# Performance work log

Hardware: AMD Instinct MI355X
Metric: run time of the kernel (lower is better)

## Reference

```python
import math
import jax, jax.numpy as jnp
import numpy as np

EMB = 768
N_HEAD = 12
B, T = 8, 1024

def setup_inputs() -> dict:
    key = jax.random.key(0)
    ks = jax.random.split(key, 5)
    x = jax.random.normal(ks[0], (B, T, EMB), dtype=jnp.float32)
    # linear params (torch nn.Linear: y = x @ W.T + b); store as [in, out] for einsum
    s1 = 1.0 / math.sqrt(EMB)
    W_attn = jax.random.uniform(ks[1], (EMB, 3 * EMB), jnp.float32, -s1, s1)
    b_attn = jax.random.uniform(ks[2], (3 * EMB,), jnp.float32, -s1, s1)
    W_proj = jax.random.uniform(ks[3], (EMB, EMB), jnp.float32, -s1, s1)
    b_proj = jax.random.uniform(ks[4], (EMB,), jnp.float32, -s1, s1)
    return {"x": x, "W_attn": W_attn, "b_attn": b_attn, "W_proj": W_proj, "b_proj": b_proj}

def reference(x, W_attn, b_attn, W_proj, b_proj):
    Bb, Tt, C = x.shape
    hd = C // N_HEAD
    qkv = x @ W_attn + b_attn                       # [B,T,3C]
    q, k, v = jnp.split(qkv, 3, axis=-1)
    # [B,T,C] -> [B,H,T,hd]
    def to_heads(t):
        return t.reshape(Bb, Tt, N_HEAD, hd).transpose(0, 2, 1, 3)
    q, k, v = to_heads(q), to_heads(k), to_heads(v)
    scale = 1.0 / math.sqrt(hd)
    scores = jnp.einsum('bhqd,bhkd->bhqk', q, k) * scale   # [B,H,T,T]
    causal = jnp.tril(jnp.ones((Tt, Tt), dtype=bool))
    scores = jnp.where(causal[None, None], scores, jnp.float32(-jnp.inf))
    attn = jax.nn.softmax(scores, axis=-1)
    y = jnp.einsum('bhqk,bhkd->bhqd', attn, v)              # [B,H,T,hd]
    y = y.transpose(0, 2, 1, 3).reshape(Bb, Tt, C)
    return y @ W_proj + b_proj
```

## Files before the change

### kernel.cpp

```cpp
#include <hip/hip_runtime.h>
#include <hip/hip_bf16.h>

typedef __hip_bfloat16 bf16;
typedef __attribute__((ext_vector_type(8))) short  bfrag;
typedef __attribute__((ext_vector_type(4))) float  facc;
typedef __attribute__((ext_vector_type(4))) short  short4v;

#define B_   8
#define T_   1024
#define C_   768
#define H_   12
#define HD_  64
#define M_   (B_ * T_)
#define N3_  (3 * C_)

#define QSCALE_ 0.18033688011112042f
#define M2_     17.312340490667562f

__device__ __forceinline__ float fexp2(float x) { return __builtin_amdgcn_exp2f(x); }

__device__ __forceinline__ void gload_lds16(const bf16* g, bf16* l) {
    __builtin_amdgcn_global_load_lds((const __attribute__((address_space(1))) void*)g,
                                     (__attribute__((address_space(3))) void*)l, 16, 0, 0);
}
__device__ __forceinline__ short bfbits(float f) {
    bf16 b = __float2bfloat16(f);
    return *reinterpret_cast<short*>(&b);
}

#define XBLK 6144
#define WABLK 1728
__global__ __launch_bounds__(256) void cvt_all_kernel(
        const float* __restrict__ x,  bf16* __restrict__ xb,
        const float* __restrict__ wa, bf16* __restrict__ wat,
        const float* __restrict__ wp, bf16* __restrict__ wpt) {
    const int bid = blockIdx.x, t = threadIdx.x;
    if (bid < XBLK) {
        const size_t i = ((size_t)bid * 256 + t) * 4;
        const float4 v = *(const float4*)(x + i);
        bf16* o = xb + i;
        o[0] = __float2bfloat16(v.x); o[1] = __float2bfloat16(v.y);
        o[2] = __float2bfloat16(v.z); o[3] = __float2bfloat16(v.w);
        return;
    }
    __shared__ float tile[32][33];
    const float* w; bf16* wt; int N, tI;
    if (bid < XBLK + WABLK) { w = wa; wt = wat; N = N3_; tI = bid - XBLK; }
    else                    { w = wp; wt = wpt; N = C_;  tI = bid - XBLK - WABLK; }
    const int ntn = N / 32;
    const int n0 = (tI % ntn) * 32, k0 = (tI / ntn) * 32;
    const int tx = t & 31, ty = t >> 5;
    for (int i = ty; i < 32; i += 8) tile[i][tx] = w[(size_t)(k0 + i) * N + n0 + tx];
    __syncthreads();
    for (int i = ty; i < 32; i += 8)
        wt[(size_t)(n0 + i) * C_ + k0 + tx] = __float2bfloat16(tile[tx][i]);
}


#define WAIT_VM(N) asm volatile("s_waitcnt vmcnt(" #N ")" ::: "memory")
#define PHASE_MID() do { __builtin_amdgcn_s_barrier();                 \
    asm volatile("s_waitcnt lgkmcnt(0)" ::: "memory");                 \
    __builtin_amdgcn_sched_barrier(0);                                 \
    __builtin_amdgcn_s_setprio(1); } while (0)
#define PHASE_END() do { __builtin_amdgcn_s_setprio(0);                \
    __builtin_amdgcn_s_barrier(); } while (0)

#define G_LOAD_A() _Pragma("unroll") for (int i = 0; i < 4; ++i) {             \
    const bf16* ar = AsC + (wrow + i * 16 + fr) * 64;                          \
    af[i][0] = *(const bfrag*)(ar + pc0);                                      \
    af[i][1] = *(const bfrag*)(ar + pc1); }

#define G_LOAD_B(CH) _Pragma("unroll") for (int j = 0; j < 2; ++j) {           \
    const bf16* br = BsC + (wcol + (CH) * 32 + j * 16 + fr) * 64;              \
    bf_[j][0] = *(const bfrag*)(br + pc0);                                     \
    bf_[j][1] = *(const bfrag*)(br + pc1); }

#define G_MFMA(CH) _Pragma("unroll") for (int i = 0; i < 4; ++i)               \
    _Pragma("unroll") for (int j = 0; j < 2; ++j) {                            \
      facc& a = acc[i][(CH) * 2 + j];                                          \
      if constexpr (SWAPPED) {                                                 \
        a = __builtin_amdgcn_mfma_f32_16x16x32_bf16(bf_[j][0], af[i][0], a, 0, 0, 0); \
        a = __builtin_amdgcn_mfma_f32_16x16x32_bf16(bf_[j][1], af[i][1], a, 0, 0, 0); \
      } else {                                                                 \
        a = __builtin_amdgcn_mfma_f32_16x16x32_bf16(af[i][0], bf_[j][0], a, 0, 0, 0); \
        a = __builtin_amdgcn_mfma_f32_16x16x32_bf16(af[i][1], bf_[j][1], a, 0, 0, 0); \
      } }

template<bool SWAPPED>
__device__ __forceinline__ void gemm192_core(
        const bf16* __restrict__ Ap, const bf16* __restrict__ Bp,
        const int m0, const int n0, bf16* smem, facc (&acc)[4][6]) {
    constexpr int KD = 768, NT = 12;
    bf16* As = smem;
    bf16* Bs = smem + 2 * 8192;
    const int t = threadIdx.x, w = t >> 6, lane = t & 63;
    const int wrow = (w >> 1) * 64;
    const int wcol = (w & 1) * 96;
    const int fr = lane & 15, quad = lane >> 4;
    const int pc0 = (quad ^ (fr & 7)) * 8;
    const int pc1 = ((quad + 4) ^ (fr & 7)) * 8;
    const int srow = t >> 3;
    const int schunk = ((t & 7) ^ (srow & 7)) * 8;
    const int sdo = srow * 64 + (t & 7) * 8;

    const bf16* Ag = Ap + (size_t)(m0 + srow) * KD + schunk;
    const bf16* Bg = Bp + (size_t)(n0 + srow) * KD + schunk;

#pragma unroll
    for (int i = 0; i < 4; ++i)
#pragma unroll
        for (int c = 0; c < 6; ++c)
#pragma unroll
            for (int r = 0; r < 4; ++r) acc[i][c][r] = 0.f;

    auto stageA = [&](bf16* dst, int k0) {
        const bf16* s = Ag + k0;
        bf16* d = dst + sdo;
#pragma unroll
        for (int r = 0; r < 4; ++r)
            gload_lds16(s + (size_t)(r * 32) * KD, d + r * 2048);
    };
    auto stageB = [&](bf16* dst, int u, int k0) {
        const bf16* s = Bg + (size_t)(u * 64) * KD + k0;
        bf16* d = dst + u * 4096 + sdo;
        gload_lds16(s, d);
        gload_lds16(s + (size_t)32 * KD, d + 2048);
    };

    stageA(As, 0);
    stageB(Bs, 0, 0); stageB(Bs, 1, 0); stageB(Bs, 2, 0);
    WAIT_VM(4);
    __builtin_amdgcn_s_barrier();

#pragma unroll 2
    for (int kt = 0; kt < NT; ++kt) {
        const int cb = kt & 1;
        const bf16* AsC = As + cb * 8192;
        const bf16* BsC = Bs + cb * 12288;
        bf16* AsN = As + (cb ^ 1) * 8192;
        bf16* BsN = Bs + (cb ^ 1) * 12288;
        const int kn = (kt + 1) * 64;
        const bool nl = kt + 1 < NT;
        bfrag af[4][2], bf_[2][2];

        G_LOAD_A();
        G_LOAD_B(0);
        if (nl) { stageA(AsN, kn); WAIT_VM(6); } else { WAIT_VM(2); }
        PHASE_MID();
        G_MFMA(0);
        PHASE_END();

        G_LOAD_B(1);
        if (nl) { stageB(BsN, 0, kn); stageB(BsN, 1, kn); WAIT_VM(8); } else { WAIT_VM(0); }
        PHASE_MID();
        G_MFMA(1);
        PHASE_END();

        G_LOAD_B(2);
        if (nl) { stageB(BsN, 2, kn); WAIT_VM(4); }
        PHASE_MID();
        G_MFMA(2);
        PHASE_END();
    }
}

__global__ __launch_bounds__(256, 2) void qkv192_kernel(
        const bf16* __restrict__ xb, const bf16* __restrict__ wat,
        const float* __restrict__ bias,
        bf16* __restrict__ Q, bf16* __restrict__ K, bf16* __restrict__ Vt) {
    extern __shared__ bf16 smem[];
    const int id = blockIdx.x;
    const int wg = (id & 7) * 96 + (id >> 3);
    const int bx = wg % 12, by = wg / 12;
    const int m0 = by * 128, n0 = bx * 192;
    const int which = n0 / C_;

    facc acc[4][6];
    if (which < 2) gemm192_core<true >(xb, wat, m0, n0, smem, acc);
    else           gemm192_core<false>(xb, wat, m0, n0, smem, acc);

    const int t = threadIdx.x, w = t >> 6, lane = t & 63;
    const int wr = (w >> 1) * 64, wc = (w & 1) * 96;
    const int fr = lane & 15, quad = lane >> 4;
    const int bb = m0 >> 10;
    if (which < 2) {
        bf16* dst = which ? K : Q;
        const float sc = which ? 1.0f : QSCALE_;
#pragma unroll
        for (int i = 0; i < 4; ++i) {
            const int tt = (m0 & 1023) + wr + i * 16 + fr;
#pragma unroll
            for (int c = 0; c < 6; ++c) {
                const int colbase = n0 + wc + c * 16 + quad * 4;
                const int cc = colbase - which * C_;
                const int h = cc >> 6, d0 = cc & 63;
                const float4 bv = *(const float4*)(bias + colbase);
                short4v pk;
                pk[0] = bfbits((acc[i][c][0] + bv.x) * sc);
                pk[1] = bfbits((acc[i][c][1] + bv.y) * sc);
                pk[2] = bfbits((acc[i][c][2] + bv.z) * sc);
                pk[3] = bfbits((acc[i][c][3] + bv.w) * sc);
                *(short4v*)(dst + ((size_t)(bb * H_ + h) * T_ + tt) * HD_ + d0) = pk;
            }
        }
    } else {
#pragma unroll
        for (int i = 0; i < 4; ++i) {
            const int tt0 = (m0 & 1023) + wr + i * 16 + quad * 4;
#pragma unroll
            for (int c = 0; c < 6; ++c) {
                const int col = n0 + wc + c * 16 + fr;
                const int cc = col - 2 * C_;
                const int h = cc >> 6, d = cc & 63;
                const float bv = bias[col];
                short4v pk;
                pk[0] = bfbits(acc[i][c][0] + bv);
                pk[1] = bfbits(acc[i][c][1] + bv);
                pk[2] = bfbits(acc[i][c][2] + bv);
                pk[3] = bfbits(acc[i][c][3] + bv);
                *(short4v*)(Vt + ((size_t)(bb * H_ + h) * HD_ + d) * T_ + tt0) = pk;
            }
        }
    }
}

__global__ __launch_bounds__(256, 2) void proj192_kernel(
        const bf16* __restrict__ y, const bf16* __restrict__ wpt,
        const float* __restrict__ bias, float* __restrict__ out) {
    extern __shared__ bf16 smem[];
    const int id = blockIdx.x;
    const int wg = (id & 7) * 32 + (id >> 3);
    const int bx = wg % 4, by = wg / 4;
    const int m0 = by * 128, n0 = bx * 192;

    facc acc[4][6];
    gemm192_core<true>(y, wpt, m0, n0, smem, acc);

    const int t = threadIdx.x, w = t >> 6, lane = t & 63;
    const int wr = (w >> 1) * 64, wc = (w & 1) * 96;
    const int fr = lane & 15, quad = lane >> 4;
#pragma unroll
    for (int i = 0; i < 4; ++i) {
        const int row = m0 + wr + i * 16 + fr;
#pragma unroll
        for (int c = 0; c < 6; ++c) {
            const int colbase = n0 + wc + c * 16 + quad * 4;
            const float4 bv = *(const float4*)(bias + colbase);
            float4 v;
            v.x = acc[i][c][0] + bv.x;
            v.y = acc[i][c][1] + bv.y;
            v.z = acc[i][c][2] + bv.z;
            v.w = acc[i][c][3] + bv.w;
            *(float4*)(out + (size_t)row * C_ + colbase) = v;
        }
    }
}

__global__ __launch_bounds__(256) void flash_attn_kernel(
        const bf16* __restrict__ Q, const bf16* __restrict__ K,
        const bf16* __restrict__ Vt, bf16* __restrict__ Y) {
    const int id   = blockIdx.x;
    const int bh   = (id & 7) * 12 + ((id >> 3) % 12);
    const int qpair = (id >> 3) / 12;
    const int t = threadIdx.x, w = t >> 6, lane = t & 63;
    const int fr = lane & 15, quad = lane >> 4, fq = quad * 8;

    __shared__ bf16 sK[2][64 * 64];
    __shared__ bf16 sVt[2][64 * 64];
    __shared__ bf16 sP[4][16][72];

    const bf16* Kbh = K  + (size_t)bh * T_ * HD_;
    const bf16* Vbh = Vt + (size_t)bh * HD_ * T_;
    const int b_ = bh / H_, h_ = bh % H_;

    const int srow = t >> 3;
    const int sgc  = ((t & 7) ^ (srow & 7)) * 8;
    const int c0   = (quad ^ (fr & 7)) * 8;

    for (int phase = 0; phase < 2; ++phase) {
        const int qt = (phase == 0) ? (15 - qpair) : qpair;
        const int q0 = qt * 64;

        const bf16* qbase = Q + ((size_t)bh * T_ + q0 + w * 16 + fr) * HD_;
        bfrag qa0 = *(const bfrag*)(qbase + fq);
        bfrag qa1 = *(const bfrag*)(qbase + 32 + fq);

        facc o[4];
        for (int nb = 0; nb < 4; ++nb) for (int r = 0; r < 4; ++r) o[nb][r] = 0.f;
        float rowl[4] = {0.f, 0.f, 0.f, 0.f};

        auto tile_step = [&](int kt, const bf16* sKp, const bf16* sVp) {
            const int k0 = kt * 64;
            facc s[4];
            for (int nb = 0; nb < 4; ++nb) for (int r = 0; r < 4; ++r) s[nb][r] = 0.f;
            for (int nb = 0; nb < 4; ++nb) {
                const bf16* kr = sKp + (nb * 16 + fr) * 64;
                bfrag kb0 = *(const bfrag*)(kr + c0);
                bfrag kb1 = *(const bfrag*)(kr + (c0 ^ 32));
                s[nb] = __builtin_amdgcn_mfma_f32_16x16x32_bf16(qa0, kb0, s[nb], 0, 0, 0);
                s[nb] = __builtin_amdgcn_mfma_f32_16x16x32_bf16(qa1, kb1, s[nb], 0, 0, 0);
            }
            const int mrow0 = q0 + w * 16 + quad * 4;
            float p[4][4];
            if (kt == qt) {
                for (int nb = 0; nb < 4; ++nb) {
                    const int n_g = k0 + nb * 16 + fr;
                    for (int r = 0; r < 4; ++r) {
                        const float a = (n_g > mrow0 + r) ? -1e30f : s[nb][r] - M2_;
                        p[nb][r] = fexp2(a);
                    }
                }
            } else {
                for (int nb = 0; nb < 4; ++nb)
                    for (int r = 0; r < 4; ++r)
                        p[nb][r] = fexp2(s[nb][r] - M2_);
            }
            for (int r = 0; r < 4; ++r)
                rowl[r] += p[0][r] + p[1][r] + p[2][r] + p[3][r];
            for (int nb = 0; nb < 4; ++nb)
                for (int r = 0; r < 4; ++r)
                    sP[w][quad * 4 + r][nb * 16 + fr] = __float2bfloat16(p[nb][r]);
            bfrag pa0 = *(const bfrag*)(&sP[w][fr][fq]);
            bfrag pa1 = *(const bfrag*)(&sP[w][fr][32 + fq]);
            for (int nb = 0; nb < 4; ++nb) {
                const bf16* vr = sVp + (nb * 16 + fr) * 64;
                bfrag vb0 = *(const bfrag*)(vr + c0);
                bfrag vb1 = *(const bfrag*)(vr + (c0 ^ 32));
                o[nb] = __builtin_amdgcn_mfma_f32_16x16x32_bf16(pa0, vb0, o[nb], 0, 0, 0);
                o[nb] = __builtin_amdgcn_mfma_f32_16x16x32_bf16(pa1, vb1, o[nb], 0, 0, 0);
            }
        };

        for (int kt = 0; kt <= qt; kt += 2) {
            const int k0 = kt * 64;
            const bool two = (kt + 1 <= qt);
            gload_lds16(Kbh + (size_t)(k0 + srow) * HD_ + sgc,      sK[0] + t * 8);
            gload_lds16(Kbh + (size_t)(k0 + 32 + srow) * HD_ + sgc, sK[0] + 2048 + t * 8);
            gload_lds16(Vbh + (size_t)srow * T_ + k0 + sgc,         sVt[0] + t * 8);
            gload_lds16(Vbh + (size_t)(srow + 32) * T_ + k0 + sgc,  sVt[0] + 2048 + t * 8);
            if (two) {
                const int k1 = k0 + 64;
                gload_lds16(Kbh + (size_t)(k1 + srow) * HD_ + sgc,      sK[1] + t * 8);
                gload_lds16(Kbh + (size_t)(k1 + 32 + srow) * HD_ + sgc, sK[1] + 2048 + t * 8);
                gload_lds16(Vbh + (size_t)srow * T_ + k1 + sgc,         sVt[1] + t * 8);
                gload_lds16(Vbh + (size_t)(srow + 32) * T_ + k1 + sgc,  sVt[1] + 2048 + t * 8);
            }
            __syncthreads();
            tile_step(kt, sK[0], sVt[0]);
            if (two) tile_step(kt + 1, sK[1], sVt[1]);
            __syncthreads();
        }

        for (int r = 0; r < 4; ++r) {
            float l = rowl[r];
            l += __shfl_xor(l, 1);
            l += __shfl_xor(l, 2);
            l += __shfl_xor(l, 4);
            l += __shfl_xor(l, 8);
            const float inv = 1.0f / l;
            const int tt = q0 + w * 16 + quad * 4 + r;
            bf16* yrow = Y + ((size_t)b_ * T_ + tt) * C_ + h_ * HD_;
            for (int nb = 0; nb < 4; ++nb)
                yrow[nb * 16 + fr] = __float2bfloat16(o[nb][r] * inv);
        }
    }
}

extern "C" void kernel_launch(void* const* d_in, const int* in_sizes, int n_in,
                              void* d_out, int out_size, void* d_ws, size_t ws_size,
                              hipStream_t stream) {
    const float* x      = (const float*)d_in[0];
    const float* W_attn = (const float*)d_in[1];
    const float* b_attn = (const float*)d_in[2];
    const float* W_proj = (const float*)d_in[3];
    const float* b_proj = (const float*)d_in[4];
    float* out = (float*)d_out;

    const size_t per = (size_t)B_ * H_ * T_ * HD_;
    bf16* Q   = (bf16*)d_ws;
    bf16* K   = Q + per;
    bf16* Vt  = K + per;
    bf16* XbY = Vt + per;
    bf16* WaT = XbY + per;
    bf16* WpT = WaT + (size_t)N3_ * C_;

    static bool s_attr = false;
    if (!s_attr) {
        hipFuncSetAttribute((const void*)qkv192_kernel,
                            hipFuncAttributeMaxDynamicSharedMemorySize, 81920);
        hipFuncSetAttribute((const void*)proj192_kernel,
                            hipFuncAttributeMaxDynamicSharedMemorySize, 81920);
        s_attr = true;
    }

    cvt_all_kernel<<<dim3(XBLK + WABLK + 576), dim3(256), 0, stream>>>(
        x, XbY, W_attn, WaT, W_proj, WpT);
    qkv192_kernel<<<dim3(768), dim3(256), 81920, stream>>>(
        XbY, WaT, b_attn, Q, K, Vt);
    flash_attn_kernel<<<dim3(768), dim3(256), 0, stream>>>(Q, K, Vt, XbY);
    proj192_kernel<<<dim3(256), dim3(256), 81920, stream>>>(
        XbY, WpT, b_proj, out);
}
```

Before: 176.2 us.

## Use 8-wave GEMM blocks with 256-row QKV tiles and rebalanced load pipeline

The shared GEMM core becomes 8-wave (512-thread) blocks, templated on rows per wave. The QKV GEMM now uses 256x192 tiles in 384 blocks, and the projection uses 128x192 tiles with half the rows per wave. Global-to-LDS staging is reorganized: all of B is issued in one phase and the wait counts are adjusted. The goal is more operand reuse per LDS tile and more waves to hide latency. The cost is 112KB of LDS for the QKV kernel, which likely limits it to one block per CU, and a fragile hand-tuned vmcnt schedule.

```diff
diff --git a/kernel.cpp b/kernel.cpp
--- a/kernel.cpp
+++ b/kernel.cpp
@@ -65,19 +65,19 @@
 #define PHASE_END() do { __builtin_amdgcn_s_setprio(0);                \
     __builtin_amdgcn_s_barrier(); } while (0)
 
-#define G_LOAD_A() _Pragma("unroll") for (int i = 0; i < 4; ++i) {             \
+#define L_A() _Pragma("unroll") for (int i = 0; i < MI; ++i) {                 \
     const bf16* ar = AsC + (wrow + i * 16 + fr) * 64;                          \
     af[i][0] = *(const bfrag*)(ar + pc0);                                      \
     af[i][1] = *(const bfrag*)(ar + pc1); }
 
-#define G_LOAD_B(CH) _Pragma("unroll") for (int j = 0; j < 2; ++j) {           \
-    const bf16* br = BsC + (wcol + (CH) * 32 + j * 16 + fr) * 64;              \
+#define L_B(P) _Pragma("unroll") for (int j = 0; j < 2; ++j) {                 \
+    const bf16* br = BsC + (wcol + ((P) * 2 + j) * 16 + fr) * 64;              \
     bf_[j][0] = *(const bfrag*)(br + pc0);                                     \
     bf_[j][1] = *(const bfrag*)(br + pc1); }
 
-#define G_MFMA(CH) _Pragma("unroll") for (int i = 0; i < 4; ++i)               \
+#define MM(P) _Pragma("unroll") for (int i = 0; i < MI; ++i)                   \
     _Pragma("unroll") for (int j = 0; j < 2; ++j) {                            \
-      facc& a = acc[i][(CH) * 2 + j];                                          \
+      facc& a = acc[i][(P) * 2 + j];                                           \
       if constexpr (SWAPPED) {                                                 \
         a = __builtin_amdgcn_mfma_f32_16x16x32_bf16(bf_[j][0], af[i][0], a, 0, 0, 0); \
         a = __builtin_amdgcn_mfma_f32_16x16x32_bf16(bf_[j][1], af[i][1], a, 0, 0, 0); \
@@ -86,28 +86,31 @@
         a = __builtin_amdgcn_mfma_f32_16x16x32_bf16(af[i][1], bf_[j][1], a, 0, 0, 0); \
       } }
 
-template<bool SWAPPED>
-__device__ __forceinline__ void gemm192_core(
+template<int MI, bool SWAPPED>
+__device__ __forceinline__ void gemm8w_core(
         const bf16* __restrict__ Ap, const bf16* __restrict__ Bp,
-        const int m0, const int n0, bf16* smem, facc (&acc)[4][6]) {
+        const int m0, const int n0, bf16* smem, facc (&acc)[MI][6]) {
     constexpr int KD = 768, NT = 12;
+    constexpr int BM  = MI * 64;
+    constexpr int LA  = MI;
+    constexpr int ASZ = BM * 64;
     bf16* As = smem;
-    bf16* Bs = smem + 2 * 8192;
+    bf16* Bs = smem + 2 * ASZ;
     const int t = threadIdx.x, w = t >> 6, lane = t & 63;
-    const int wrow = (w >> 1) * 64;
+    const int wrow = (w >> 1) * (MI * 16);
     const int wcol = (w & 1) * 96;
     const int fr = lane & 15, quad = lane >> 4;
     const int pc0 = (quad ^ (fr & 7)) * 8;
     const int pc1 = ((quad + 4) ^ (fr & 7)) * 8;
     const int srow = t >> 3;
     const int schunk = ((t & 7) ^ (srow & 7)) * 8;
-    const int sdo = srow * 64 + (t & 7) * 8;
+    const int sdo = t * 8;
 
     const bf16* Ag = Ap + (size_t)(m0 + srow) * KD + schunk;
     const bf16* Bg = Bp + (size_t)(n0 + srow) * KD + schunk;
 
 #pragma unroll
-    for (int i = 0; i < 4; ++i)
+    for (int i = 0; i < MI; ++i)
 #pragma unroll
         for (int c = 0; c < 6; ++c)
 #pragma unroll
@@ -117,67 +120,73 @@
         const bf16* s = Ag + k0;
         bf16* d = dst + sdo;
 #pragma unroll
-        for (int r = 0; r < 4; ++r)
-            gload_lds16(s + (size_t)(r * 32) * KD, d + r * 2048);
+        for (int r = 0; r < LA; ++r)
+            gload_lds16(s + (size_t)(r * 64) * KD, d + r * 4096);
     };
-    auto stageB = [&](bf16* dst, int u, int k0) {
-        const bf16* s = Bg + (size_t)(u * 64) * KD + k0;
-        bf16* d = dst + u * 4096 + sdo;
-        gload_lds16(s, d);
-        gload_lds16(s + (size_t)32 * KD, d + 2048);
+    auto stageB = [&](bf16* dst, int k0) {
+        const bf16* s = Bg + k0;
+        bf16* d = dst + sdo;
+#pragma unroll
+        for (int r = 0; r < 3; ++r)
+            gload_lds16(s + (size_t)(r * 64) * KD, d + r * 4096);
     };
 
     stageA(As, 0);
-    stageB(Bs, 0, 0); stageB(Bs, 1, 0); stageB(Bs, 2, 0);
-    WAIT_VM(4);
+    stageB(Bs, 0);
+    WAIT_VM(0);
     __builtin_amdgcn_s_barrier();
 
 #pragma unroll 2
     for (int kt = 0; kt < NT; ++kt) {
         const int cb = kt & 1;
-        const bf16* AsC = As + cb * 8192;
+        const bf16* AsC = As + cb * ASZ;
         const bf16* BsC = Bs + cb * 12288;
-        bf16* AsN = As + (cb ^ 1) * 8192;
+        bf16* AsN = As + (cb ^ 1) * ASZ;
         bf16* BsN = Bs + (cb ^ 1) * 12288;
         const int kn = (kt + 1) * 64;
         const bool nl = kt + 1 < NT;
-        bfrag af[4][2], bf_[2][2];
-
-        G_LOAD_A();
-        G_LOAD_B(0);
-        if (nl) { stageA(AsN, kn); WAIT_VM(6); } else { WAIT_VM(2); }
+        bfrag af[MI][2], bf_[2][2];
+
+        L_A();
+        L_B(0);
+        if (nl) {
+            stageA(AsN, kn);
+            if constexpr (MI == 4) WAIT_VM(4); else WAIT_VM(2);
+        } else {
+            WAIT_VM(0);
+        }
         PHASE_MID();
-        G_MFMA(0);
+        MM(0);
         PHASE_END();
 
-        G_LOAD_B(1);
-        if (nl) { stageB(BsN, 0, kn); stageB(BsN, 1, kn); WAIT_VM(8); } else { WAIT_VM(0); }
+        L_B(1);
+        if (nl) stageB(BsN, kn);
         PHASE_MID();
-        G_MFMA(1);
+        MM(1);
         PHASE_END();
 
-        G_LOAD_B(2);
-        if (nl) { stageB(BsN, 2, kn); WAIT_VM(4); }
+        L_B(2);
+        if (nl) WAIT_VM(1);
         PHASE_MID();
-        G_MFMA(2);
+        MM(2);
         PHASE_END();
     }
 }
 
-__global__ __launch_bounds__(256, 2) void qkv192_kernel(
+__global__ __launch_bounds__(512, 2) void qkv8_kernel(
         const bf16* __restrict__ xb, const bf16* __restrict__ wat,
         const float* __restrict__ bias,
         bf16* __restrict__ Q, bf16* __restrict__ K, bf16* __restrict__ Vt) {
     extern __shared__ bf16 smem[];
     const int id = blockIdx.x;
-    const int wg = (id & 7) * 96 + (id >> 3);
+    const int wg = (id & 7) * 48 + (id >> 3);
     const int bx = wg % 12, by = wg / 12;
-    const int m0 = by * 128, n0 = bx * 192;
+    const int m0 = by * 256, n0 = bx * 192;
     const int which = n0 / C_;
 
     facc acc[4][6];
-    if (which < 2) gemm192_core<true >(xb, wat, m0, n0, smem, acc);
-    else           gemm192_core<false>(xb, wat, m0, n0, smem, acc);
+    if (which < 2) gemm8w_core<4, true >(xb, wat, m0, n0, smem, acc);
+    else           gemm8w_core<4, false>(xb, wat, m0, n0, smem, acc);
 
     const int t = threadIdx.x, w = t >> 6, lane = t & 63;
     const int wr = (w >> 1) * 64, wc = (w & 1) * 96;
@@ -224,7 +233,7 @@
     }
 }
 
-__global__ __launch_bounds__(256, 2) void proj192_kernel(
+__global__ __launch_bounds__(512, 2) void proj8_kernel(
         const bf16* __restrict__ y, const bf16* __restrict__ wpt,
         const float* __restrict__ bias, float* __restrict__ out) {
     extern __shared__ bf16 smem[];
@@ -233,14 +242,14 @@
     const int bx = wg % 4, by = wg / 4;
     const int m0 = by * 128, n0 = bx * 192;
 
-    facc acc[4][6];
-    gemm192_core<true>(y, wpt, m0, n0, smem, acc);
+    facc acc[2][6];
+    gemm8w_core<2, true>(y, wpt, m0, n0, smem, acc);
 
     const int t = threadIdx.x, w = t >> 6, lane = t & 63;
-    const int wr = (w >> 1) * 64, wc = (w & 1) * 96;
+    const int wr = (w >> 1) * 32, wc = (w & 1) * 96;
     const int fr = lane & 15, quad = lane >> 4;
 #pragma unroll
-    for (int i = 0; i < 4; ++i) {
+    for (int i = 0; i < 2; ++i) {
         const int row = m0 + wr + i * 16 + fr;
 #pragma unroll
         for (int c = 0; c < 6; ++c) {
@@ -386,18 +395,18 @@
 
     static bool s_attr = false;
     if (!s_attr) {
-        hipFuncSetAttribute((const void*)qkv192_kernel,
-                            hipFuncAttributeMaxDynamicSharedMemorySize, 81920);
-        hipFuncSetAttribute((const void*)proj192_kernel,
+        hipFuncSetAttribute((const void*)qkv8_kernel,
+                            hipFuncAttributeMaxDynamicSharedMemorySize, 114688);
+        hipFuncSetAttribute((const void*)proj8_kernel,
                             hipFuncAttributeMaxDynamicSharedMemorySize, 81920);
         s_attr = true;
     }
 
     cvt_all_kernel<<<dim3(XBLK + WABLK + 576), dim3(256), 0, stream>>>(
         x, XbY, W_attn, WaT, W_proj, WpT);
-    qkv192_kernel<<<dim3(768), dim3(256), 81920, stream>>>(
+    qkv8_kernel<<<dim3(384), dim3(512), 114688, stream>>>(
         XbY, WaT, b_attn, Q, K, Vt);
     flash_attn_kernel<<<dim3(768), dim3(256), 0, stream>>>(Q, K, Vt, XbY);
-    proj192_kernel<<<dim3(256), dim3(256), 81920, stream>>>(
+    proj8_kernel<<<dim3(256), dim3(512), 81920, stream>>>(
         XbY, WpT, b_proj, out);
 }
```

After: 184.2 us. 1.05x slower.

## Replace phased GEMM pipeline with simple double-buffered loop and syncthreads

Applied to the files above, without the earlier changes.

Replaces the three-phase GEMM mainloop, which interleaved partial LDS staging with fine-grained vmcnt waits, barriers and setprio, with a plain double-buffered loop. Each iteration issues the full next A/B tile loads, computes all 6 column chunks, then does a single __syncthreads. This simplifies scheduling but gives up the explicit interleaving of loads with MFMA phases. It also relies on __syncthreads to wait for the async LDS loads.

```diff
diff --git a/kernel.cpp b/kernel.cpp
--- a/kernel.cpp
+++ b/kernel.cpp
@@ -57,37 +57,8 @@
 }
 
 
-#define WAIT_VM(N) asm volatile("s_waitcnt vmcnt(" #N ")" ::: "memory")
-#define PHASE_MID() do { __builtin_amdgcn_s_barrier();                 \
-    asm volatile("s_waitcnt lgkmcnt(0)" ::: "memory");                 \
-    __builtin_amdgcn_sched_barrier(0);                                 \
-    __builtin_amdgcn_s_setprio(1); } while (0)
-#define PHASE_END() do { __builtin_amdgcn_s_setprio(0);                \
-    __builtin_amdgcn_s_barrier(); } while (0)
-
-#define G_LOAD_A() _Pragma("unroll") for (int i = 0; i < 4; ++i) {             \
-    const bf16* ar = AsC + (wrow + i * 16 + fr) * 64;                          \
-    af[i][0] = *(const bfrag*)(ar + pc0);                                      \
-    af[i][1] = *(const bfrag*)(ar + pc1); }
-
-#define G_LOAD_B(CH) _Pragma("unroll") for (int j = 0; j < 2; ++j) {           \
-    const bf16* br = BsC + (wcol + (CH) * 32 + j * 16 + fr) * 64;              \
-    bf_[j][0] = *(const bfrag*)(br + pc0);                                     \
-    bf_[j][1] = *(const bfrag*)(br + pc1); }
-
-#define G_MFMA(CH) _Pragma("unroll") for (int i = 0; i < 4; ++i)               \
-    _Pragma("unroll") for (int j = 0; j < 2; ++j) {                            \
-      facc& a = acc[i][(CH) * 2 + j];                                          \
-      if constexpr (SWAPPED) {                                                 \
-        a = __builtin_amdgcn_mfma_f32_16x16x32_bf16(bf_[j][0], af[i][0], a, 0, 0, 0); \
-        a = __builtin_amdgcn_mfma_f32_16x16x32_bf16(bf_[j][1], af[i][1], a, 0, 0, 0); \
-      } else {                                                                 \
-        a = __builtin_amdgcn_mfma_f32_16x16x32_bf16(af[i][0], bf_[j][0], a, 0, 0, 0); \
-        a = __builtin_amdgcn_mfma_f32_16x16x32_bf16(af[i][1], bf_[j][1], a, 0, 0, 0); \
-      } }
-
 template<bool SWAPPED>
-__device__ __forceinline__ void gemm192_core(
+__device__ __forceinline__ void gemm_db_core(
         const bf16* __restrict__ Ap, const bf16* __restrict__ Bp,
         const int m0, const int n0, bf16* smem, facc (&acc)[4][6]) {
     constexpr int KD = 768, NT = 12;
@@ -101,7 +72,7 @@
     const int pc1 = ((quad + 4) ^ (fr & 7)) * 8;
     const int srow = t >> 3;
     const int schunk = ((t & 7) ^ (srow & 7)) * 8;
-    const int sdo = srow * 64 + (t & 7) * 8;
+    const int sdo = t * 8;
 
     const bf16* Ag = Ap + (size_t)(m0 + srow) * KD + schunk;
     const bf16* Bg = Bp + (size_t)(n0 + srow) * KD + schunk;
@@ -120,51 +91,55 @@
         for (int r = 0; r < 4; ++r)
             gload_lds16(s + (size_t)(r * 32) * KD, d + r * 2048);
     };
-    auto stageB = [&](bf16* dst, int u, int k0) {
-        const bf16* s = Bg + (size_t)(u * 64) * KD + k0;
-        bf16* d = dst + u * 4096 + sdo;
-        gload_lds16(s, d);
-        gload_lds16(s + (size_t)32 * KD, d + 2048);
+    auto stageB = [&](bf16* dst, int k0) {
+        const bf16* s = Bg + k0;
+        bf16* d = dst + sdo;
+#pragma unroll
+        for (int r = 0; r < 6; ++r)
+            gload_lds16(s + (size_t)(r * 32) * KD, d + r * 2048);
     };
 
     stageA(As, 0);
-    stageB(Bs, 0, 0); stageB(Bs, 1, 0); stageB(Bs, 2, 0);
-    WAIT_VM(4);
-    __builtin_amdgcn_s_barrier();
+    stageB(Bs, 0);
+    __syncthreads();
 
 #pragma unroll 2
     for (int kt = 0; kt < NT; ++kt) {
         const int cb = kt & 1;
         const bf16* AsC = As + cb * 8192;
         const bf16* BsC = Bs + cb * 12288;
-        bf16* AsN = As + (cb ^ 1) * 8192;
-        bf16* BsN = Bs + (cb ^ 1) * 12288;
-        const int kn = (kt + 1) * 64;
-        const bool nl = kt + 1 < NT;
-        bfrag af[4][2], bf_[2][2];
-
-        G_LOAD_A();
-        G_LOAD_B(0);
-        if (nl) { stageA(AsN, kn); WAIT_VM(6); } else { WAIT_VM(2); }
-        PHASE_MID();
-        G_MFMA(0);
-        PHASE_END();
-
-        G_LOAD_B(1);
-        if (nl) { stageB(BsN, 0, kn); stageB(BsN, 1, kn); WAIT_VM(8); } else { WAIT_VM(0); }
-        PHASE_MID();
-        G_MFMA(1);
-        PHASE_END();
-
-        G_LOAD_B(2);
-        if (nl) { stageB(BsN, 2, kn); WAIT_VM(4); }
-        PHASE_MID();
-        G_MFMA(2);
-        PHASE_END();
-    }
-}
-
-__global__ __launch_bounds__(256, 2) void qkv192_kernel(
+        if (kt + 1 < NT) {
+            stageA(As + (cb ^ 1) * 8192,  (kt + 1) * 64);
+            stageB(Bs + (cb ^ 1) * 12288, (kt + 1) * 64);
+        }
+        bfrag af[4][2];
+#pragma unroll
+        for (int i = 0; i < 4; ++i) {
+            const bf16* ar = AsC + (wrow + i * 16 + fr) * 64;
+            af[i][0] = *(const bfrag*)(ar + pc0);
+            af[i][1] = *(const bfrag*)(ar + pc1);
+        }
+#pragma unroll
+        for (int c = 0; c < 6; ++c) {
+            const bf16* br = BsC + (wcol + c * 16 + fr) * 64;
+            bfrag b0 = *(const bfrag*)(br + pc0);
+            bfrag b1 = *(const bfrag*)(br + pc1);
+#pragma unroll
+            for (int i = 0; i < 4; ++i) {
+                if constexpr (SWAPPED) {
+                    acc[i][c] = __builtin_amdgcn_mfma_f32_16x16x32_bf16(b0, af[i][0], acc[i][c], 0, 0, 0);
+                    acc[i][c] = __builtin_amdgcn_mfma_f32_16x16x32_bf16(b1, af[i][1], acc[i][c], 0, 0, 0);
+                } else {
+                    acc[i][c] = __builtin_amdgcn_mfma_f32_16x16x32_bf16(af[i][0], b0, acc[i][c], 0, 0, 0);
+                    acc[i][c] = __builtin_amdgcn_mfma_f32_16x16x32_bf16(af[i][1], b1, acc[i][c], 0, 0, 0);
+                }
+            }
+        }
+        __syncthreads();
+    }
+}
+
+__global__ __launch_bounds__(256, 2) void qkv_db_kernel(
         const bf16* __restrict__ xb, const bf16* __restrict__ wat,
         const float* __restrict__ bias,
         bf16* __restrict__ Q, bf16* __restrict__ K, bf16* __restrict__ Vt) {
@@ -176,8 +151,8 @@
     const int which = n0 / C_;
 
     facc acc[4][6];
-    if (which < 2) gemm192_core<true >(xb, wat, m0, n0, smem, acc);
-    else           gemm192_core<false>(xb, wat, m0, n0, smem, acc);
+    if (which < 2) gemm_db_core<true >(xb, wat, m0, n0, smem, acc);
+    else           gemm_db_core<false>(xb, wat, m0, n0, smem, acc);
 
     const int t = threadIdx.x, w = t >> 6, lane = t & 63;
     const int wr = (w >> 1) * 64, wc = (w & 1) * 96;
@@ -224,7 +199,7 @@
     }
 }
 
-__global__ __launch_bounds__(256, 2) void proj192_kernel(
+__global__ __launch_bounds__(256, 2) void proj_db_kernel(
         const bf16* __restrict__ y, const bf16* __restrict__ wpt,
         const float* __restrict__ bias, float* __restrict__ out) {
     extern __shared__ bf16 smem[];
@@ -234,7 +209,7 @@
     const int m0 = by * 128, n0 = bx * 192;
 
     facc acc[4][6];
-    gemm192_core<true>(y, wpt, m0, n0, smem, acc);
+    gemm_db_core<true>(y, wpt, m0, n0, smem, acc);
 
     const int t = threadIdx.x, w = t >> 6, lane = t & 63;
     const int wr = (w >> 1) * 64, wc = (w & 1) * 96;
@@ -386,18 +361,18 @@
 
     static bool s_attr = false;
     if (!s_attr) {
-        hipFuncSetAttribute((const void*)qkv192_kernel,
+        hipFuncSetAttribute((const void*)qkv_db_kernel,
                             hipFuncAttributeMaxDynamicSharedMemorySize, 81920);
-        hipFuncSetAttribute((const void*)proj192_kernel,
+        hipFuncSetAttribute((const void*)proj_db_kernel,
                             hipFuncAttributeMaxDynamicSharedMemorySize, 81920);
         s_attr = true;
     }
 
     cvt_all_kernel<<<dim3(XBLK + WABLK + 576), dim3(256), 0, stream>>>(
         x, XbY, W_attn, WaT, W_proj, WpT);
-    qkv192_kernel<<<dim3(768), dim3(256), 81920, stream>>>(
+    qkv_db_kernel<<<dim3(768), dim3(256), 81920, stream>>>(
         XbY, WaT, b_attn, Q, K, Vt);
     flash_attn_kernel<<<dim3(768), dim3(256), 0, stream>>>(Q, K, Vt, XbY);
-    proj192_kernel<<<dim3(256), dim3(256), 81920, stream>>>(
+    proj_db_kernel<<<dim3(256), dim3(256), 81920, stream>>>(
         XbY, WpT, b_proj, out);
 }
```

After: 175.8 us. Within noise of the previous version (-0.2%).
